# Kernel optimization log

Measured on AMD Instinct MI355X. Metric: run time of the kernel, lower is better.

Reference implementation:

```python
import jax, jax.numpy as jnp
import numpy as np

B, T, V, E, H, C = 64, 512, 50257, 128, 64, 20

def _lstm_params(key, in_dim, scale=0.05):
    k1, k2, k3 = jax.random.split(key, 3)
    return (jax.random.normal(k1, (in_dim, 4 * H)) * scale,
            jax.random.normal(k2, (H, 4 * H)) * scale,
            jax.random.normal(k3, (4 * H,)) * scale)

def setup_inputs():
    key = jax.random.key(0)
    ks = jax.random.split(key, 10)
    lengths = jax.random.randint(ks[0], (B,), T // 4, T + 1)
    mask = (jnp.arange(T)[None, :] < lengths[:, None]).astype(jnp.int32)
    ids = jax.random.randint(ks[1], (B, T), 1, V) * mask  # pad id 0 past length
    positions = jnp.broadcast_to(jnp.arange(T, dtype=jnp.int32), (B, T))
    x = jnp.stack([ids, positions, mask], axis=1)  # [B,3,T]
    inp = {"x": x,
           "word_emb": jax.random.normal(ks[2], (V, E)) * 0.05,
           "pos_emb": jax.random.normal(ks[3], (V, E)) * 0.05}
    for name, in_dim, kk in [("f0", E, ks[4]), ("f1", H, ks[5]), ("b0", E, ks[6]), ("b1", H, ks[7])]:
        Wx, Wh, b = _lstm_params(kk, in_dim)
        inp["wx_" + name] = Wx
        inp["wh_" + name] = Wh
        inp["b_" + name] = b
    inp["dense_w"] = jax.random.normal(ks[8], (H, C)) * 0.05
    inp["dense_b"] = jnp.zeros((C,), jnp.float32)
    return inp

def _lstm_layer(xs, mask, Wx, Wh, b, backwards):
    # xs: [B,T,D], mask: [B,T] bool. Keras masking semantics: at masked steps
    # hidden/cell state (and emitted output) carry over from the previous step.
    # go_backwards reverses inputs AND mask, and does NOT re-reverse outputs
    # (that is the raw keras LSTM behaviour without the Bidirectional wrapper).
    if backwards:
        xs = xs[:, ::-1]
        mask = mask[:, ::-1]
    xT = jnp.swapaxes(xs, 0, 1)    # [T,B,D]
    mT = jnp.swapaxes(mask, 0, 1)  # [T,B]
    h0 = jnp.zeros((xs.shape[0], H), xs.dtype)
    c0 = h0
    def step(carry, inp):
        h, c = carry
        x_t, m_t = inp
        z = x_t @ Wx + h @ Wh + b  # [B,4H], keras gate order i,f,g,o
        i = jax.nn.sigmoid(z[:, :H])
        f = jax.nn.sigmoid(z[:, H:2 * H])
        g = jnp.tanh(z[:, 2 * H:3 * H])
        o = jax.nn.sigmoid(z[:, 3 * H:])
        c_new = f * c + i * g
        h_new = o * jnp.tanh(c_new)
        m = m_t[:, None]
        h2 = jnp.where(m, h_new, h)
        c2 = jnp.where(m, c_new, c)
        return (h2, c2), h2
    _, hs = jax.lax.scan(step, (h0, c0), (xT, mT))
    return jnp.swapaxes(hs, 0, 1)  # [B,T,H]

def reference(x, word_emb, pos_emb, wx_f0, wh_f0, b_f0, wx_f1, wh_f1, b_f1,
              wx_b0, wh_b0, b_b0, wx_b1, wh_b1, b_b1, dense_w, dense_b):
    ids, positions, attn = x[:, 0, :], x[:, 1, :], x[:, 2, :]
    mask = attn.astype(bool)
    emb = word_emb[ids] + pos_emb[positions]  # [B,T,E]
    f = _lstm_layer(emb, mask, wx_f0, wh_f0, b_f0, False)
    f = _lstm_layer(f, mask, wx_f1, wh_f1, b_f1, False)
    bo = _lstm_layer(emb, mask, wx_b0, wh_b0, b_b0, True)
    bo = _lstm_layer(bo, mask, wx_b1, wh_b1, b_b1, True)
    # Concatenate(axis=1) stacks [fwd_out, bwd_out] along TIME, dense+softmax
    # per step, then [:, -1, :] -> only the last step of the backward stack
    # reaches the output (faithful to the original module).
    last = bo[:, -1, :]
    return jax.nn.softmax(last @ dense_w + dense_b, axis=-1)  # [B,C]
```

## Files before the change

kernel.cpp:

```cpp
#include <hip/hip_runtime.h>
#include <hip/hip_bf16.h>

#define Bn 64
#define Tn 512
#define En 128
#define Hn 64
#define Gn 256
#define Cn 20

__device__ __forceinline__ float sigf(float x)      { return 1.f/(1.f+__expf(-x)); }
__device__ __forceinline__ float tanhfast(float x)  { return 2.f/(1.f+__expf(-2.f*x)) - 1.f; }

__global__ __launch_bounds__(256, 1) void emb_proj_kernel(
    const int* __restrict__ x, const float* __restrict__ word_emb,
    const float* __restrict__ pos_emb, const float* __restrict__ wx,
    const float* __restrict__ bias, float* __restrict__ z0)
{
  __shared__ float emb[64][En];
  __shared__ float wxl[32][Gn];
  const int tid  = threadIdx.x;
  const int row0 = blockIdx.x * 64;

  #pragma unroll
  for (int it = 0; it < 8; ++it) {
    int idx = it*256 + tid;
    int rr  = idx >> 5;
    int e4  = (idx & 31) << 2;
    int r   = row0 + rr;
    int b   = r >> 9;
    int t   = r & (Tn-1);
    int id  = x[b*3*Tn + t];
    float4 we = *reinterpret_cast<const float4*>(&word_emb[(size_t)id*En + e4]);
    float4 pe = *reinterpret_cast<const float4*>(&pos_emb[(size_t)t*En + e4]);
    *reinterpret_cast<float4*>(&emb[rr][e4]) =
        make_float4(we.x+pe.x, we.y+pe.y, we.z+pe.z, we.w+pe.w);
  }

  const int jc = tid & 63;
  const int rg = tid >> 6;
  float acc[16][4];
  float4 bb = *reinterpret_cast<const float4*>(&bias[jc*4]);
  #pragma unroll
  for (int r = 0; r < 16; ++r) { acc[r][0]=bb.x; acc[r][1]=bb.y; acc[r][2]=bb.z; acc[r][3]=bb.w; }

  for (int ec = 0; ec < 4; ++ec) {
    __syncthreads();
    #pragma unroll
    for (int it = 0; it < 8; ++it) {
      int idx = it*256 + tid;
      int ee  = idx >> 6;
      int j4  = (idx & 63) << 2;
      *reinterpret_cast<float4*>(&wxl[ee][j4]) =
          *reinterpret_cast<const float4*>(&wx[(size_t)(ec*32+ee)*Gn + j4]);
    }
    __syncthreads();
    for (int ee = 0; ee < 32; ++ee) {
      float4 w = *reinterpret_cast<const float4*>(&wxl[ee][jc*4]);
      #pragma unroll
      for (int r = 0; r < 16; ++r) {
        float xv = emb[rg*16+r][ec*32+ee];
        acc[r][0] = fmaf(xv, w.x, acc[r][0]);
        acc[r][1] = fmaf(xv, w.y, acc[r][1]);
        acc[r][2] = fmaf(xv, w.z, acc[r][2]);
        acc[r][3] = fmaf(xv, w.w, acc[r][3]);
      }
    }
  }
  #pragma unroll
  for (int r = 0; r < 16; ++r) {
    size_t row = (size_t)row0 + rg*16 + r;
    *reinterpret_cast<float4*>(&z0[row*Gn + jc*4]) =
        make_float4(acc[r][0], acc[r][1], acc[r][2], acc[r][3]);
  }
}

__global__ __launch_bounds__(256, 1) void zx1_gemm_kernel(
    const float* __restrict__ hb0, const float* __restrict__ wx,
    const float* __restrict__ bias, float* __restrict__ zx1)
{
  __shared__ float xl[64][Hn];
  __shared__ float wl[32][Gn];
  const int tid  = threadIdx.x;
  const int row0 = blockIdx.x * 64;

  #pragma unroll
  for (int it = 0; it < 4; ++it) {
    int idx = it*256 + tid;
    int rr  = idx >> 4;
    int e4  = (idx & 15) << 2;
    *reinterpret_cast<float4*>(&xl[rr][e4]) =
        *reinterpret_cast<const float4*>(&hb0[((size_t)row0+rr)*Hn + e4]);
  }

  const int jc = tid & 63;
  const int rg = tid >> 6;
  float acc[16][4];
  float4 bb = *reinterpret_cast<const float4*>(&bias[jc*4]);
  #pragma unroll
  for (int r = 0; r < 16; ++r) { acc[r][0]=bb.x; acc[r][1]=bb.y; acc[r][2]=bb.z; acc[r][3]=bb.w; }

  for (int kc = 0; kc < 2; ++kc) {
    __syncthreads();
    #pragma unroll
    for (int it = 0; it < 8; ++it) {
      int idx = it*256 + tid;
      int kk  = idx >> 6;
      int j4  = (idx & 63) << 2;
      *reinterpret_cast<float4*>(&wl[kk][j4]) =
          *reinterpret_cast<const float4*>(&wx[(size_t)(kc*32+kk)*Gn + j4]);
    }
    __syncthreads();
    for (int kk = 0; kk < 32; ++kk) {
      float4 w = *reinterpret_cast<const float4*>(&wl[kk][jc*4]);
      #pragma unroll
      for (int r = 0; r < 16; ++r) {
        float xv = xl[rg*16+r][kc*32+kk];
        acc[r][0] = fmaf(xv, w.x, acc[r][0]);
        acc[r][1] = fmaf(xv, w.y, acc[r][1]);
        acc[r][2] = fmaf(xv, w.z, acc[r][2]);
        acc[r][3] = fmaf(xv, w.w, acc[r][3]);
      }
    }
  }
  #pragma unroll
  for (int r = 0; r < 16; ++r) {
    size_t row = (size_t)row0 + rg*16 + r;
    *reinterpret_cast<float4*>(&zx1[row*Gn + jc*4]) =
        make_float4(acc[r][0], acc[r][1], acc[r][2], acc[r][3]);
  }
}

#define WAVE_BARRIER()                                        \
  do {                                                        \
    asm volatile("s_waitcnt lgkmcnt(0)" ::: "memory");        \
    __builtin_amdgcn_sched_barrier(0);                        \
    __builtin_amdgcn_s_barrier();                             \
    __builtin_amdgcn_sched_barrier(0);                        \
  } while (0)

template<bool IS_B0>
__global__ __launch_bounds__(256, 1) void lstm_fast(
    const int* __restrict__ x, const float* __restrict__ z,
    const float* __restrict__ wh, float* __restrict__ hb0,
    const float* __restrict__ dw, const float* __restrict__ db,
    float* __restrict__ out)
{
  const int b   = blockIdx.x;
  const int tid = threadIdx.x;
  const int wv  = tid >> 6;
  const int l   = tid & 63;

  __shared__ __align__(16) float z_s[2][Gn];
  __shared__ __align__(16) float h_own[4][Hn];
  __shared__ float sm[2][32];
  __shared__ int msk[Tn];

  float wcol[Hn];
  #pragma unroll
  for (int k = 0; k < Hn; ++k) wcol[k] = wh[(size_t)k*Gn + tid];

  for (int i = tid; i < Tn; i += 256) msk[i] = x[b*3*Tn + 2*Tn + i];
  h_own[wv][l] = 0.f;
  float c = 0.f, h = 0.f;
  const float* zr   = z + (size_t)b*Tn*Gn;
  float*       hout = hb0 + (size_t)b*Tn*Hn;
  __syncthreads();

  float zpA, zpB, zpC, zpD;
  {
    int t0 = IS_B0 ? Tn-1 : 0;
    int t1 = IS_B0 ? Tn-2 : 1;
    int t2 = IS_B0 ? Tn-3 : 2;
    int t3 = IS_B0 ? Tn-4 : 3;
    zpA = zr[(size_t)t0*Gn + tid];
    zpB = zr[(size_t)t1*Gn + tid];
    zpC = zr[(size_t)t2*Gn + tid];
    zpD = zr[(size_t)t3*Gn + tid];
  }

#define STEP(s_, ZREG)                                                       \
  {                                                                          \
    const int t_ = IS_B0 ? (Tn-1-(s_)) : (s_);                               \
    const int mi = IS_B0 ? t_ : (Tn-1-t_);                                   \
    if (msk[mi]) {                                                           \
      float a0 = ZREG, a1 = 0.f, a2 = 0.f, a3 = 0.f;                         \
      _Pragma("unroll")                                                      \
      for (int k4 = 0; k4 < Hn/4; ++k4) {                                    \
        float4 hv = *reinterpret_cast<const float4*>(&h_own[wv][k4*4]);      \
        a0 = fmaf(hv.x, wcol[k4*4+0], a0);                                   \
        a1 = fmaf(hv.y, wcol[k4*4+1], a1);                                   \
        a2 = fmaf(hv.z, wcol[k4*4+2], a2);                                   \
        a3 = fmaf(hv.w, wcol[k4*4+3], a3);                                   \
      }                                                                      \
      z_s[(s_)&1][tid] = (a0+a1)+(a2+a3);                                    \
      WAVE_BARRIER();                                                        \
      float g0 = z_s[(s_)&1][l];                                             \
      float g1 = z_s[(s_)&1][Hn+l];                                          \
      float g2 = z_s[(s_)&1][2*Hn+l];                                        \
      float g3 = z_s[(s_)&1][3*Hn+l];                                        \
      float ig = sigf(g0), fg = sigf(g1);                                    \
      float gg = tanhfast(g2), og = sigf(g3);                                \
      c = fmaf(fg, c, ig*gg);                                                \
      h = og * tanhfast(c);                                                  \
      h_own[wv][l] = h;                                                      \
    }                                                                        \
    if (IS_B0 && wv == 0) hout[(size_t)t_*Hn + l] = h;                       \
    {                                                                        \
      int tn_ = IS_B0 ? (t_-4) : (t_+4);                                     \
      tn_ = tn_ < 0 ? 0 : (tn_ > Tn-1 ? Tn-1 : tn_);                         \
      ZREG = zr[(size_t)tn_*Gn + tid];                                       \
    }                                                                        \
  }

  for (int s = 0; s < Tn; s += 4) {
    STEP(s+0, zpA);
    STEP(s+1, zpB);
    STEP(s+2, zpC);
    STEP(s+3, zpD);
  }
#undef STEP

  if (!IS_B0) {
    if (tid < Cn) {
      float lg = db[tid];
      #pragma unroll
      for (int k = 0; k < Hn; ++k) lg = fmaf(h_own[0][k], dw[k*Cn + tid], lg);
      sm[0][tid] = lg;
    }
    if (tid < Cn) {
      float m = sm[0][0];
      #pragma unroll
      for (int k = 1; k < Cn; ++k) m = fmaxf(m, sm[0][k]);
      float e = __expf(sm[0][tid] - m);
      sm[1][tid] = e;
      float ssum = 0.f;
      #pragma unroll
      for (int k = 0; k < Cn; ++k) ssum += sm[1][k];
      out[b*Cn + tid] = e / ssum;
    }
  }
}

extern "C" void kernel_launch(void* const* d_in, const int* in_sizes, int n_in,
                              void* d_out, int out_size, void* d_ws, size_t ws_size,
                              hipStream_t stream)
{
  const int*   x        = (const int*)  d_in[0];
  const float* word_emb = (const float*)d_in[1];
  const float* pos_emb  = (const float*)d_in[2];
  const float* wx_b0    = (const float*)d_in[9];
  const float* wh_b0    = (const float*)d_in[10];
  const float* b_b0     = (const float*)d_in[11];
  const float* wx_b1    = (const float*)d_in[12];
  const float* wh_b1    = (const float*)d_in[13];
  const float* b_b1     = (const float*)d_in[14];
  const float* dw       = (const float*)d_in[15];
  const float* db       = (const float*)d_in[16];
  float* out = (float*)d_out;

  float* z0  = (float*)d_ws;
  float* hb0 = z0 + (size_t)Bn*Tn*Gn;

  emb_proj_kernel<<<dim3((Bn*Tn)/64), dim3(256), 0, stream>>>(
      x, word_emb, pos_emb, wx_b0, b_b0, z0);
  lstm_fast<true><<<dim3(Bn), dim3(256), 0, stream>>>(
      x, z0, wh_b0, hb0, nullptr, nullptr, nullptr);
  zx1_gemm_kernel<<<dim3((Bn*Tn)/64), dim3(256), 0, stream>>>(
      hb0, wx_b1, b_b1, z0);
  lstm_fast<false><<<dim3(Bn), dim3(256), 0, stream>>>(
      x, z0, wh_b1, hb0, dw, db, out);
}
```

Measured before the change: 693.9 us.

## Run LSTM recurrence only over valid length and stream gate inputs via LDS ring

Computes each sequence's valid length with an atomic sum over the mask and iterates only over the masked-in steps, relying on the contiguous prefix mask structure. This skips the padded steps entirely, and it also removes the per-step mask branch. Per-step gate-input prefetches now use global_load_lds into a 4-slot LDS ring with explicit vmcnt waits instead of register prefetches. The loop now assumes the mask is a contiguous prefix, and the hand-tuned vmcnt counts (including dummy loads to pad the counter) are fragile. Padded positions of the hb0 output are no longer written in the b0 pass.

```diff
diff --git a/kernel.cpp b/kernel.cpp
--- a/kernel.cpp
+++ b/kernel.cpp
@@ -138,6 +138,11 @@
     __builtin_amdgcn_sched_barrier(0);                        \
   } while (0)
 
+#define GLDS(ldsptr, gptr)                                            \
+  __builtin_amdgcn_global_load_lds(                                   \
+      (const __attribute__((address_space(1))) void*)(gptr),          \
+      (__attribute__((address_space(3))) void*)(ldsptr), 4, 0, 0)
+
 template<bool IS_B0>
 __global__ __launch_bounds__(256, 1) void lstm_fast(
     const int* __restrict__ x, const float* __restrict__ z,
@@ -152,73 +157,81 @@
 
   __shared__ __align__(16) float z_s[2][Gn];
   __shared__ __align__(16) float h_own[4][Hn];
+  __shared__ __align__(16) float ring[4][Gn];
   __shared__ float sm[2][32];
-  __shared__ int msk[Tn];
-
+  __shared__ int slen;
+
+  if (tid == 0) slen = 0;
+  __syncthreads();
+  {
+    int m0 = x[b*3*Tn + 2*Tn + tid];
+    int m1 = x[b*3*Tn + 2*Tn + 256 + tid];
+    atomicAdd(&slen, m0 + m1);
+  }
   float wcol[Hn];
   #pragma unroll
   for (int k = 0; k < Hn; ++k) wcol[k] = wh[(size_t)k*Gn + tid];
-
-  for (int i = tid; i < Tn; i += 256) msk[i] = x[b*3*Tn + 2*Tn + i];
   h_own[wv][l] = 0.f;
+  __syncthreads();
+  const int len = slen;
+
+  const float* zr   = z   + (size_t)b*Tn*Gn;
+  float*       hout = hb0 + (size_t)b*Tn*Hn;
   float c = 0.f, h = 0.f;
-  const float* zr   = z + (size_t)b*Tn*Gn;
-  float*       hout = hb0 + (size_t)b*Tn*Hn;
-  __syncthreads();
-
-  float zpA, zpB, zpC, zpD;
-  {
-    int t0 = IS_B0 ? Tn-1 : 0;
-    int t1 = IS_B0 ? Tn-2 : 1;
-    int t2 = IS_B0 ? Tn-3 : 2;
-    int t3 = IS_B0 ? Tn-4 : 3;
-    zpA = zr[(size_t)t0*Gn + tid];
-    zpB = zr[(size_t)t1*Gn + tid];
-    zpC = zr[(size_t)t2*Gn + tid];
-    zpD = zr[(size_t)t3*Gn + tid];
-  }
-
-#define STEP(s_, ZREG)                                                       \
-  {                                                                          \
-    const int t_ = IS_B0 ? (Tn-1-(s_)) : (s_);                               \
-    const int mi = IS_B0 ? t_ : (Tn-1-t_);                                   \
-    if (msk[mi]) {                                                           \
-      float a0 = ZREG, a1 = 0.f, a2 = 0.f, a3 = 0.f;                         \
-      _Pragma("unroll")                                                      \
-      for (int k4 = 0; k4 < Hn/4; ++k4) {                                    \
-        float4 hv = *reinterpret_cast<const float4*>(&h_own[wv][k4*4]);      \
-        a0 = fmaf(hv.x, wcol[k4*4+0], a0);                                   \
-        a1 = fmaf(hv.y, wcol[k4*4+1], a1);                                   \
-        a2 = fmaf(hv.z, wcol[k4*4+2], a2);                                   \
-        a3 = fmaf(hv.w, wcol[k4*4+3], a3);                                   \
-      }                                                                      \
-      z_s[(s_)&1][tid] = (a0+a1)+(a2+a3);                                    \
-      WAVE_BARRIER();                                                        \
-      float g0 = z_s[(s_)&1][l];                                             \
-      float g1 = z_s[(s_)&1][Hn+l];                                          \
-      float g2 = z_s[(s_)&1][2*Hn+l];                                        \
-      float g3 = z_s[(s_)&1][3*Hn+l];                                        \
-      float ig = sigf(g0), fg = sigf(g1);                                    \
-      float gg = tanhfast(g2), og = sigf(g3);                                \
-      c = fmaf(fg, c, ig*gg);                                                \
-      h = og * tanhfast(c);                                                  \
-      h_own[wv][l] = h;                                                      \
-    }                                                                        \
-    if (IS_B0 && wv == 0) hout[(size_t)t_*Hn + l] = h;                       \
-    {                                                                        \
-      int tn_ = IS_B0 ? (t_-4) : (t_+4);                                     \
-      tn_ = tn_ < 0 ? 0 : (tn_ > Tn-1 ? Tn-1 : tn_);                         \
-      ZREG = zr[(size_t)tn_*Gn + tid];                                       \
-    }                                                                        \
-  }
-
-  for (int s = 0; s < Tn; s += 4) {
-    STEP(s+0, zpA);
-    STEP(s+1, zpB);
-    STEP(s+2, zpC);
-    STEP(s+3, zpD);
-  }
-#undef STEP
+
+  const int t0 = IS_B0 ? (len - 1) : (Tn - len);
+
+  GLDS(&ring[0][wv*64], zr + (size_t)t0*Gn + tid);
+  GLDS(&ring[1][wv*64], zr + (size_t)(IS_B0 ? t0-1 : t0+1)*Gn + tid);
+  GLDS(&ring[2][wv*64], zr + (size_t)(IS_B0 ? t0-2 : t0+2)*Gn + tid);
+  GLDS(&ring[3][wv*64], zr + (size_t)(IS_B0 ? t0-3 : t0+3)*Gn + tid);
+  GLDS(&ring[0][wv*64], zr + (size_t)t0*Gn + tid);
+  GLDS(&ring[0][wv*64], zr + (size_t)t0*Gn + tid);
+  GLDS(&ring[0][wv*64], zr + (size_t)t0*Gn + tid);
+  asm volatile("s_waitcnt vmcnt(3)" ::: "memory");
+  __builtin_amdgcn_sched_barrier(0);
+  float zcur = ring[0][tid];
+
+  for (int s = 0; s < len; ++s) {
+    const int t = IS_B0 ? (len-1-s) : (Tn-len+s);
+
+    float a0 = zcur, a1 = 0.f, a2 = 0.f, a3 = 0.f;
+    #pragma unroll
+    for (int k4 = 0; k4 < 16; ++k4) {
+      float4 hv = *reinterpret_cast<const float4*>(&h_own[wv][k4*4]);
+      a0 = fmaf(hv.x, wcol[k4*4+0], a0);
+      a1 = fmaf(hv.y, wcol[k4*4+1], a1);
+      a2 = fmaf(hv.z, wcol[k4*4+2], a2);
+      a3 = fmaf(hv.w, wcol[k4*4+3], a3);
+    }
+    z_s[s&1][tid] = (a0+a1)+(a2+a3);
+    WAVE_BARRIER();
+
+    if (IS_B0 && wv == 0) { asm volatile("s_waitcnt vmcnt(4)" ::: "memory"); }
+    else                  { asm volatile("s_waitcnt vmcnt(2)" ::: "memory"); }
+    __builtin_amdgcn_sched_barrier(0);
+    float znext = ring[(s+1)&3][tid];
+
+    float g0 = z_s[s&1][l],      g1 = z_s[s&1][Hn+l];
+    float g2 = z_s[s&1][2*Hn+l], g3 = z_s[s&1][3*Hn+l];
+    float ig = sigf(g0), fg = sigf(g1);
+    float gg = tanhfast(g2), og = sigf(g3);
+    c = fmaf(fg, c, ig*gg);
+    h = og * tanhfast(c);
+    h_own[wv][l] = h;
+
+    if (IS_B0 && wv == 0) {
+      const float* sp = hout + (size_t)t*Hn + l;
+      asm volatile("global_store_dword %0, %1, off" :: "v"(sp), "v"(h));
+    }
+
+    {
+      int tn = IS_B0 ? (t-4) : (t+4);
+      tn = tn < 0 ? 0 : (tn > Tn-1 ? Tn-1 : tn);
+      GLDS(&ring[s&3][wv*64], zr + (size_t)tn*Gn + tid);
+    }
+    zcur = znext;
+  }
 
   if (!IS_B0) {
     if (tid < Cn) {
```

Result: slower. 832.3 us (+19.9%).
